# Performance work log

Measured on AMD Instinct MI355X. Metric: run time of the kernel, lower is better.

The kernel has to match this reference:

```python
import jax, jax.numpy as jnp
import numpy as np

OUT_SL = 32


def gru_cell(x, h, Wih, Whh, bih, bhh):
    # PyTorch GRU cell: gates ordered (r, z, n)
    gi = x @ Wih.T + bih
    gh = h @ Whh.T + bhh
    ir, iz, inn = jnp.split(gi, 3, axis=-1)
    hr, hz, hn = jnp.split(gh, 3, axis=-1)
    r = jax.nn.sigmoid(ir + hr)
    z = jax.nn.sigmoid(iz + hz)
    n = jnp.tanh(inn + r * hn)
    return (1.0 - z) * n + z * h


def run_gru_layer(xs, h0, Wih, Whh, bih, bhh, reverse=False):
    def step(h, x):
        h = gru_cell(x, h, Wih, Whh, bih, bhh)
        return h, h
    hT, ys = jax.lax.scan(step, h0, xs, reverse=reverse)
    return ys, hT


def setup_inputs() -> dict:
    key = jax.random.key(0)
    ks = iter(jax.random.split(key, 32))

    def p(shape, fan_in):
        return (jax.random.normal(next(ks), shape, dtype=jnp.float32)
                / np.sqrt(fan_in).astype(np.float32))

    V_ENC, V_DEC, EE, ED, NH = 32000, 32000, 300, 300, 256
    inp = jax.random.randint(next(ks), (128, 64), 0, V_ENC)
    return {
        'emb_enc': p((V_ENC, EE), 1.0),
        'enc_Wih0': p((2, 3 * NH, EE), EE),
        'enc_Whh0': p((2, 3 * NH, NH), NH),
        'enc_bih0': p((2, 3 * NH), NH),
        'enc_bhh0': p((2, 3 * NH), NH),
        'enc_Wih1': p((2, 3 * NH, 2 * NH), 2 * NH),
        'enc_Whh1': p((2, 3 * NH, NH), NH),
        'enc_bih1': p((2, 3 * NH), NH),
        'enc_bhh1': p((2, 3 * NH), NH),
        'W_out_enc': p((ED, 2 * NH), 2 * NH),
        'emb_dec': p((V_DEC, ED), 1.0),
        'dec_Wih': p((2, 3 * ED, ED), ED),
        'dec_Whh': p((2, 3 * ED, ED), ED),
        'dec_bih': p((2, 3 * ED), ED),
        'dec_bhh': p((2, 3 * ED), ED),
        'W1': p((2 * NH, ED), 2 * NH),
        'l2_W': p((ED, ED), ED),
        'l2_b': p((ED,), ED),
        'l3_W': p((ED, ED + 2 * NH), ED + 2 * NH),
        'l3_b': p((ED,), ED),
        'V_att': p((ED,), ED),
        'out_b': p((V_DEC,), ED),
        'inp': inp,
    }


def reference(emb_enc, enc_Wih0, enc_Whh0, enc_bih0, enc_bhh0,
              enc_Wih1, enc_Whh1, enc_bih1, enc_bhh1, W_out_enc,
              emb_dec, dec_Wih, dec_Whh, dec_bih, dec_bhh,
              W1, l2_W, l2_b, l3_W, l3_b, V_att, out_b, inp):
    sl, bs = inp.shape
    nh = enc_Whh0.shape[-1]
    h0 = jnp.zeros((bs, nh), dtype=emb_enc.dtype)

    # ---- encoder: 2-layer bidirectional GRU (dropout in eval mode = identity)
    emb = emb_enc[inp]                                        # (sl, bs, EE)
    yf0, hf0 = run_gru_layer(emb, h0, enc_Wih0[0], enc_Whh0[0], enc_bih0[0], enc_bhh0[0])
    yb0, hb0 = run_gru_layer(emb, h0, enc_Wih0[1], enc_Whh0[1], enc_bih0[1], enc_bhh0[1], reverse=True)
    x1 = jnp.concatenate([yf0, yb0], axis=-1)                 # (sl, bs, 2*nh)
    yf1, hf1 = run_gru_layer(x1, h0, enc_Wih1[0], enc_Whh1[0], enc_bih1[0], enc_bhh1[0])
    yb1, hb1 = run_gru_layer(x1, h0, enc_Wih1[1], enc_Whh1[1], enc_bih1[1], enc_bhh1[1], reverse=True)
    enc_out = jnp.concatenate([yf1, yb1], axis=-1)            # (sl, bs, 2*nh)

    # h.view(2,2,bs,-1).permute(0,2,1,3) -> concat fwd/bwd per layer
    h = jnp.stack([jnp.concatenate([hf0, hb0], axis=-1),
                   jnp.concatenate([hf1, hb1], axis=-1)])     # (2, bs, 2*nh)
    h = h @ W_out_enc.T                                       # (2, bs, ED)

    w1e = enc_out @ W1                                        # (sl, bs, ED)
    dec_inp0 = jnp.zeros((bs,), dtype=jnp.int32)

    def dec_step(carry, _):
        h, dec_inp = carry
        w2h = h[-1] @ l2_W.T + l2_b                           # (bs, ED)
        u = jnp.tanh(w1e + w2h[None])                         # (sl, bs, ED)
        a = jax.nn.softmax(u @ V_att, axis=0)                 # (sl, bs), softmax over seq
        Xa = jnp.einsum('sb,sbd->bd', a, enc_out)             # (bs, 2*nh)
        e = emb_dec[dec_inp]                                  # (bs, ED)
        x = jnp.concatenate([e, Xa], axis=1) @ l3_W.T + l3_b  # (bs, ED)
        h0n = gru_cell(x, h[0], dec_Wih[0], dec_Whh[0], dec_bih[0], dec_bhh[0])
        h1n = gru_cell(h0n, h[1], dec_Wih[1], dec_Whh[1], dec_bih[1], dec_bhh[1])
        outp = h1n @ emb_dec.T + out_b                        # (bs, V_dec), tied weights
        ndec = jnp.argmax(outp, axis=1).astype(jnp.int32)
        return (jnp.stack([h0n, h1n]), ndec), outp

    (_, _), res = jax.lax.scan(dec_step, (h, dec_inp0), None, length=OUT_SL)
    return res                                                # (out_sl, bs, V_dec)
```

## Files before the change

kernel.cpp:

```cpp
#include <hip/hip_runtime.h>
#include <math.h>


#define DINL static __device__ __forceinline__

DINL float sigm(float x) { return 1.0f / (1.0f + expf(-x)); }
DINL float dot4f(float4 a, float4 b) { return a.x*b.x + a.y*b.y + a.z*b.z + a.w*b.w; }

__global__ __launch_bounds__(256) void k_embed(const float4* __restrict__ E,
                                               const int* __restrict__ inp,
                                               float4* __restrict__ out) {
  int i = blockIdx.x * 256 + threadIdx.x;
  if (i >= 8192 * 75) return;
  int row = i / 75, q = i - row * 75;
  out[i] = E[(size_t)inp[row] * 75 + q];
}

__global__ __launch_bounds__(256) void k_transpose(const float* __restrict__ A,
                                                   float* __restrict__ B, int R, int C) {
  __shared__ float tile[32][33];
  int c0 = blockIdx.x * 32, r0 = blockIdx.y * 32;
  int tx = threadIdx.x & 31, ty = threadIdx.x >> 5;
  for (int i = 0; i < 32; i += 8) {
    int r = r0 + ty + i, c = c0 + tx;
    if (r < R && c < C) tile[ty + i][tx] = A[(size_t)r * C + c];
  }
  __syncthreads();
  for (int i = 0; i < 32; i += 8) {
    int c = c0 + ty + i, r = r0 + tx;
    if (c < C && r < R) B[(size_t)c * R + r] = tile[tx][ty + i];
  }
}

__global__ __launch_bounds__(256) void k_gemm_nt(const float* __restrict__ A,
                                                 const float* __restrict__ B,
                                                 const float* __restrict__ bias,
                                                 float* __restrict__ C,
                                                 int N, int M, int K) {
  __shared__ float As[16][65];
  __shared__ float Bs[16][65];
  const int tid = threadIdx.x;
  const int bn = blockIdx.x * 64, bm = blockIdx.y * 64;
  const int tn = (tid >> 4) << 2, tm = (tid & 15) << 2;
  float acc[4][4] = {};
  for (int k0 = 0; k0 < K; k0 += 16) {
    for (int i = tid; i < 1024; i += 256) {
      int kk = i & 15, n = i >> 4;
      int gk = k0 + kk;
      As[kk][n] = (gk < K) ? A[(size_t)(bn + n) * K + gk] : 0.0f;
      Bs[kk][n] = (gk < K && (bm + n) < M) ? B[(size_t)(bm + n) * K + gk] : 0.0f;
    }
    __syncthreads();
#pragma unroll
    for (int kk = 0; kk < 16; ++kk) {
      float a[4], bb[4];
#pragma unroll
      for (int i = 0; i < 4; ++i) a[i] = As[kk][tn + i];
#pragma unroll
      for (int j = 0; j < 4; ++j) bb[j] = Bs[kk][tm + j];
#pragma unroll
      for (int i = 0; i < 4; ++i)
#pragma unroll
        for (int j = 0; j < 4; ++j) acc[i][j] += a[i] * bb[j];
    }
    __syncthreads();
  }
#pragma unroll
  for (int i = 0; i < 4; ++i) {
    int row = bn + tn + i;
#pragma unroll
    for (int j = 0; j < 4; ++j) {
      int col = bm + tm + j;
      if (row < N && col < M)
        C[(size_t)row * M + col] = acc[i][j] + (bias ? bias[col] : 0.0f);
    }
  }
}

__global__ __launch_bounds__(256) void k_enc_step(
    const float* __restrict__ giF, const float* __restrict__ giB,
    const float* __restrict__ hinF, const float* __restrict__ hinB,
    float* __restrict__ houtF, float* __restrict__ houtB,
    const float* __restrict__ WhhF, const float* __restrict__ WhhB,
    const float* __restrict__ bhhF, const float* __restrict__ bhhB,
    float* __restrict__ yF, float* __restrict__ yB) {
  const int dir = blockIdx.z;
  const float* gi = dir ? giB : giF;
  const float* hin = dir ? hinB : hinF;
  float* hout = dir ? houtB : houtF;
  const float* Whh = dir ? WhhB : WhhF;
  const float* bhh = dir ? bhhB : bhhF;
  float* y = dir ? yB : yF;
  const int ycol = dir ? 256 : 0;

  const int c0 = blockIdx.x * 16;
  const int b0 = blockIdx.y * 16;
  const int tid = threadIdx.x;
  const int cl = tid & 15, bl = tid >> 4;

  __shared__ __align__(16) float Wlds[3][16][260];
  for (int i = tid; i < 48 * 64; i += 256) {
    int row = i >> 6, q = i & 63;
    int g = row >> 4, rc = row & 15;
    float4 w = ((const float4*)Whh)[(size_t)(c0 + rc + (g << 8)) * 64 + q];
    *(float4*)&Wlds[g][rc][q << 2] = w;
  }
  __syncthreads();

  const int b = b0 + bl;
  const int c = c0 + cl;
  const float* hrow = hin + (b << 8);
  float ar = 0.f, az = 0.f, an = 0.f;
#pragma unroll 4
  for (int k = 0; k < 256; k += 4) {
    float4 hv = *(const float4*)(hrow + k);
    float4 wr = *(const float4*)&Wlds[0][cl][k];
    float4 wz = *(const float4*)&Wlds[1][cl][k];
    float4 wn = *(const float4*)&Wlds[2][cl][k];
    ar += dot4f(hv, wr);
    az += dot4f(hv, wz);
    an += dot4f(hv, wn);
  }
  float ghr = ar + bhh[c], ghz = az + bhh[256 + c], ghn = an + bhh[512 + c];
  const float* gir = gi + (size_t)b * 768;
  float r = sigm(gir[c] + ghr);
  float z = sigm(gir[256 + c] + ghz);
  float n = tanhf(gir[512 + c] + r * ghn);
  float hold = hrow[c];
  float hnew = (1.f - z) * n + z * hold;
  hout[(b << 8) + c] = hnew;
  y[(b << 9) + ycol + c] = hnew;
}

__global__ __launch_bounds__(256) void k_hcat(const float* __restrict__ x1,
                                              const float* __restrict__ encout,
                                              float* __restrict__ hcat) {
  int i = blockIdx.x * 256 + threadIdx.x;
  int l = i >> 15, r = i & 32767, b = r >> 9, d = r & 511;
  const float* src = l ? encout : x1;
  int ts = (d < 256) ? 127 : 0;
  hcat[i] = src[((size_t)(ts << 6) + b) * 512 + d];
}

__global__ __launch_bounds__(256) void k_dec_att(
    const float* __restrict__ h1, const float* __restrict__ w1e,
    const float* __restrict__ encout,
    const float* __restrict__ l2W, const float* __restrict__ l2b,
    const float* __restrict__ l3W, const float* __restrict__ l3b,
    const float* __restrict__ Vatt, const float* __restrict__ embdec,
    const int* __restrict__ decin, float* __restrict__ xdec) {
  const int b = blockIdx.x, tid = threadIdx.x;
  __shared__ __align__(16) float h1s[300];
  __shared__ __align__(16) float w2h[300];
  __shared__ __align__(16) float eXa[812];
  __shared__ float aa[128];
  __shared__ float red[128];

  for (int i = tid; i < 300; i += 256) h1s[i] = h1[b * 300 + i];
  __syncthreads();

  for (int m = tid; m < 300; m += 256) {
    const float4* wr = (const float4*)(l2W + (size_t)m * 300);
    const float4* hr = (const float4*)h1s;
    float acc = l2b[m];
    for (int q = 0; q < 75; ++q) acc += dot4f(wr[q], hr[q]);
    w2h[m] = acc;
  }
  __syncthreads();

  if (tid < 128) {
    const float4* wp = (const float4*)(w1e + ((size_t)(tid << 6) + b) * 300);
    const float4* vp = (const float4*)Vatt;
    const float4* hp = (const float4*)w2h;
    float acc = 0.f;
    for (int q = 0; q < 75; ++q) {
      float4 w = wp[q], h = hp[q], v = vp[q];
      acc += tanhf(w.x + h.x) * v.x + tanhf(w.y + h.y) * v.y +
             tanhf(w.z + h.z) * v.z + tanhf(w.w + h.w) * v.w;
    }
    aa[tid] = acc;
    red[tid] = acc;
  }
  __syncthreads();
  for (int s = 64; s > 0; s >>= 1) {
    if (tid < s) red[tid] = fmaxf(red[tid], red[tid + s]);
    __syncthreads();
  }
  float mx = red[0];
  __syncthreads();
  if (tid < 128) {
    float ex = expf(aa[tid] - mx);
    aa[tid] = ex;
    red[tid] = ex;
  }
  __syncthreads();
  for (int s = 64; s > 0; s >>= 1) {
    if (tid < s) red[tid] += red[tid + s];
    __syncthreads();
  }
  float inv = 1.0f / red[0];
  __syncthreads();
  if (tid < 128) aa[tid] *= inv;
  int ib = decin[b];
  for (int d = tid; d < 300; d += 256) eXa[d] = embdec[(size_t)ib * 300 + d];
  __syncthreads();

  for (int d = tid; d < 512; d += 256) {
    float acc = 0.f;
    for (int s = 0; s < 128; ++s) acc += aa[s] * encout[((size_t)(s << 6) + b) * 512 + d];
    eXa[300 + d] = acc;
  }
  __syncthreads();

  for (int m = tid; m < 300; m += 256) {
    const float4* wr = (const float4*)(l3W + (size_t)m * 812);
    const float4* xr = (const float4*)eXa;
    float acc = l3b[m];
    for (int q = 0; q < 203; ++q) acc += dot4f(wr[q], xr[q]);
    xdec[b * 300 + m] = acc;
  }
}

__global__ __launch_bounds__(256) void k_gru300(
    const float* __restrict__ xin, const float* __restrict__ hin,
    float* __restrict__ hout, float* __restrict__ houtT,
    const float* __restrict__ Wih, const float* __restrict__ Whh,
    const float* __restrict__ bih, const float* __restrict__ bhh) {
  const int tid = threadIdx.x;
  const int cl = tid & 15, bl = tid >> 4;
  const int c = blockIdx.x * 16 + cl;
  const int b0 = blockIdx.y * 16;
  const int b = b0 + bl;
  __shared__ __align__(16) float xs[16][300];
  __shared__ __align__(16) float hs[16][300];
  for (int i = tid; i < 16 * 75; i += 256) {
    int row = i / 75, q = i - row * 75;
    ((float4*)&xs[row][0])[q] = ((const float4*)(xin + (size_t)(b0 + row) * 300))[q];
    ((float4*)&hs[row][0])[q] = ((const float4*)(hin + (size_t)(b0 + row) * 300))[q];
  }
  __syncthreads();
  if (c < 300) {
    float gir = bih[c], giz = bih[300 + c], gin = bih[600 + c];
    float ghr = bhh[c], ghz = bhh[300 + c], ghn = bhh[600 + c];
    const float4* wir = (const float4*)(Wih + (size_t)c * 300);
    const float4* wiz = (const float4*)(Wih + (size_t)(300 + c) * 300);
    const float4* win = (const float4*)(Wih + (size_t)(600 + c) * 300);
    const float4* whr = (const float4*)(Whh + (size_t)c * 300);
    const float4* whz = (const float4*)(Whh + (size_t)(300 + c) * 300);
    const float4* whn = (const float4*)(Whh + (size_t)(600 + c) * 300);
    const float4* xr = (const float4*)&xs[bl][0];
    const float4* hr = (const float4*)&hs[bl][0];
    for (int q = 0; q < 75; ++q) {
      float4 xv = xr[q], hv = hr[q];
      gir += dot4f(xv, wir[q]);
      giz += dot4f(xv, wiz[q]);
      gin += dot4f(xv, win[q]);
      ghr += dot4f(hv, whr[q]);
      ghz += dot4f(hv, whz[q]);
      ghn += dot4f(hv, whn[q]);
    }
    float r = sigm(gir + ghr), z = sigm(giz + ghz);
    float n = tanhf(gin + r * ghn);
    float hnew = (1.f - z) * n + z * hs[bl][c];
    hout[(size_t)b * 300 + c] = hnew;
    if (houtT) houtT[(size_t)c * 64 + b] = hnew;
  }
}

__global__ __launch_bounds__(256) void k_dec_out(const float* __restrict__ embT,
                                                 const float* __restrict__ h1T,
                                                 const float* __restrict__ outb,
                                                 float* __restrict__ out) {
  const int v = blockIdx.x * 256 + threadIdx.x;
  const int bh = blockIdx.y;
  const float* h = h1T + bh * 32;
  float acc[32];
#pragma unroll
  for (int i = 0; i < 32; ++i) acc[i] = 0.f;
  for (int k = 0; k < 300; ++k) {
    float ev = embT[(size_t)k * 32000 + v];
#pragma unroll
    for (int i = 0; i < 32; ++i) acc[i] += ev * h[(size_t)k * 64 + i];
  }
  float bo = outb[v];
#pragma unroll
  for (int i = 0; i < 32; ++i) out[(size_t)(bh * 32 + i) * 32000 + v] = acc[i] + bo;
}

__global__ __launch_bounds__(256) void k_argmax(const float* __restrict__ out,
                                                int* __restrict__ decin) {
  const int b = blockIdx.x, tid = threadIdx.x;
  const float* row = out + (size_t)b * 32000;
  float best = -INFINITY;
  int bi = 0;
  for (int v = tid; v < 32000; v += 256) {
    float x = row[v];
    if (x > best) { best = x; bi = v; }
  }
  __shared__ float bv[256];
  __shared__ int bidx[256];
  bv[tid] = best;
  bidx[tid] = bi;
  __syncthreads();
  for (int s = 128; s > 0; s >>= 1) {
    if (tid < s) {
      if (bv[tid + s] > bv[tid] || (bv[tid + s] == bv[tid] && bidx[tid + s] < bidx[tid])) {
        bv[tid] = bv[tid + s];
        bidx[tid] = bidx[tid + s];
      }
    }
    __syncthreads();
  }
  if (tid == 0) decin[b] = bidx[0];
}

extern "C" void kernel_launch(void* const* d_in, const int* in_sizes, int n_in,
                              void* d_out_v, int out_size, void* d_ws, size_t ws_size,
                              hipStream_t stream) {
  (void)in_sizes; (void)n_in; (void)out_size; (void)ws_size;
  const float* emb_enc = (const float*)d_in[0];
  const float* eWih0   = (const float*)d_in[1];
  const float* eWhh0   = (const float*)d_in[2];
  const float* ebih0   = (const float*)d_in[3];
  const float* ebhh0   = (const float*)d_in[4];
  const float* eWih1   = (const float*)d_in[5];
  const float* eWhh1   = (const float*)d_in[6];
  const float* ebih1   = (const float*)d_in[7];
  const float* ebhh1   = (const float*)d_in[8];
  const float* Wout    = (const float*)d_in[9];
  const float* emb_dec = (const float*)d_in[10];
  const float* dWih    = (const float*)d_in[11];
  const float* dWhh    = (const float*)d_in[12];
  const float* dbih    = (const float*)d_in[13];
  const float* dbhh    = (const float*)d_in[14];
  const float* W1      = (const float*)d_in[15];
  const float* l2W     = (const float*)d_in[16];
  const float* l2b     = (const float*)d_in[17];
  const float* l3W     = (const float*)d_in[18];
  const float* l3b     = (const float*)d_in[19];
  const float* Vatt    = (const float*)d_in[20];
  const float* outb    = (const float*)d_in[21];
  const int* inp       = (const int*)d_in[22];
  float* d_out = (float*)d_out_v;

  float* ws = (float*)d_ws;
  size_t off = 0;
  auto take = [&](size_t n) { float* p = ws + off; off += (n + 3) & ~(size_t)3; return p; };
  float* embT   = take((size_t)300 * 32000);
  float* encout = take((size_t)8192 * 512);
  float* w1e    = take((size_t)8192 * 300);
  float* W1T    = take((size_t)300 * 512);
  float* hcat   = take((size_t)128 * 512);
  float* dech   = take((size_t)2 * 2 * 64 * 300);
  float* h1T    = take((size_t)300 * 64);
  float* xdec   = take((size_t)64 * 300);
  float* henc   = take((size_t)4 * 64 * 256);
  int* decin    = (int*)take(64);

  float* emb  = d_out;
  float* gi0f = emb + 2457600;
  float* gi0b = gi0f + 6291456;
  float* x1   = gi0b + 6291456;
  float* gi1f = x1 + 4194304;
  float* gi1b = gi1f + 6291456;

  k_embed<<<2400, 256, 0, stream>>>((const float4*)emb_enc, inp, (float4*)emb);
  k_transpose<<<dim3(10, 16), 256, 0, stream>>>(W1, W1T, 512, 300);
  k_transpose<<<dim3(10, 1000), 256, 0, stream>>>(emb_dec, embT, 32000, 300);

  k_gemm_nt<<<dim3(128, 12), 256, 0, stream>>>(emb, eWih0, ebih0, gi0f, 8192, 768, 300);
  k_gemm_nt<<<dim3(128, 12), 256, 0, stream>>>(emb, eWih0 + 230400, ebih0 + 768, gi0b, 8192, 768, 300);
  hipMemsetAsync(henc, 0, 4 * 64 * 256 * sizeof(float), stream);
  for (int t = 0; t < 128; ++t) {
    int tb = 127 - t, pp = t & 1, np = pp ^ 1;
    k_enc_step<<<dim3(16, 4, 2), 256, 0, stream>>>(
        gi0f + (size_t)t * 49152, gi0b + (size_t)tb * 49152,
        henc + (pp * 2 + 0) * 16384, henc + (pp * 2 + 1) * 16384,
        henc + (np * 2 + 0) * 16384, henc + (np * 2 + 1) * 16384,
        eWhh0, eWhh0 + 196608, ebhh0, ebhh0 + 768,
        x1 + (size_t)t * 32768, x1 + (size_t)tb * 32768);
  }

  k_gemm_nt<<<dim3(128, 12), 256, 0, stream>>>(x1, eWih1, ebih1, gi1f, 8192, 768, 512);
  k_gemm_nt<<<dim3(128, 12), 256, 0, stream>>>(x1, eWih1 + 393216, ebih1 + 768, gi1b, 8192, 768, 512);
  hipMemsetAsync(henc, 0, 4 * 64 * 256 * sizeof(float), stream);
  for (int t = 0; t < 128; ++t) {
    int tb = 127 - t, pp = t & 1, np = pp ^ 1;
    k_enc_step<<<dim3(16, 4, 2), 256, 0, stream>>>(
        gi1f + (size_t)t * 49152, gi1b + (size_t)tb * 49152,
        henc + (pp * 2 + 0) * 16384, henc + (pp * 2 + 1) * 16384,
        henc + (np * 2 + 0) * 16384, henc + (np * 2 + 1) * 16384,
        eWhh1, eWhh1 + 196608, ebhh1, ebhh1 + 768,
        encout + (size_t)t * 32768, encout + (size_t)tb * 32768);
  }

  k_hcat<<<256, 256, 0, stream>>>(x1, encout, hcat);
  k_gemm_nt<<<dim3(2, 5), 256, 0, stream>>>(hcat, Wout, nullptr, dech, 128, 300, 512);
  k_gemm_nt<<<dim3(128, 5), 256, 0, stream>>>(encout, W1T, nullptr, w1e, 8192, 300, 512);

  hipMemsetAsync(decin, 0, 64 * sizeof(int), stream);
  for (int t = 0; t < 32; ++t) {
    int cur = t & 1, nxt = cur ^ 1;
    float* hc = dech + cur * 38400;
    float* hn = dech + nxt * 38400;
    k_dec_att<<<64, 256, 0, stream>>>(hc + 19200, w1e, encout, l2W, l2b, l3W, l3b,
                                      Vatt, emb_dec, decin, xdec);
    k_gru300<<<dim3(19, 4), 256, 0, stream>>>(xdec, hc, hn, nullptr,
                                              dWih, dWhh, dbih, dbhh);
    k_gru300<<<dim3(19, 4), 256, 0, stream>>>(hn, hc + 19200, hn + 19200, h1T,
                                              dWih + 270000, dWhh + 270000,
                                              dbih + 900, dbhh + 900);
    k_dec_out<<<dim3(125, 2), 256, 0, stream>>>(embT, h1T, outb,
                                                d_out + (size_t)t * 2048000);
    k_argmax<<<64, 256, 0, stream>>>(d_out + (size_t)t * 2048000, decin);
  }
}
```

Baseline: 11.22 ms.

## Persistent encoder recurrence with grid barriers, larger GEMM tiles, fused argmax

Replaces 128 per-timestep encoder launches per layer with one persistent kernel per layer. Blocks sharing a batch slice synchronise each step through atomic counters in global memory. The input-projection GEMM moves to 128x128 tiles with 8x8 register blocking, and the separate argmax kernel is folded into the output projection via packed 64-bit max keys reduced in the next attention kernel. This removes launch overhead and a full re-read of the logits, but relies on all 128 blocks being co-resident, which spin barriers require.

```diff
diff --git a/kernel.cpp b/kernel.cpp
--- a/kernel.cpp
+++ b/kernel.cpp
@@ -6,6 +6,15 @@
 
 DINL float sigm(float x) { return 1.0f / (1.0f + expf(-x)); }
 DINL float dot4f(float4 a, float4 b) { return a.x*b.x + a.y*b.y + a.z*b.z + a.w*b.w; }
+
+DINL unsigned long long packmax(float x, int v) {
+  unsigned u = __float_as_uint(x);
+  u = (u & 0x80000000u) ? ~u : (u | 0x80000000u);
+  return ((unsigned long long)u << 32) | (unsigned)(~v);
+}
+DINL unsigned long long umax64(unsigned long long a, unsigned long long b) {
+  return a > b ? a : b;
+}
 
 __global__ __launch_bounds__(256) void k_embed(const float4* __restrict__ E,
                                                const int* __restrict__ inp,
@@ -32,104 +41,123 @@
   }
 }
 
-__global__ __launch_bounds__(256) void k_gemm_nt(const float* __restrict__ A,
+__global__ __launch_bounds__(256) void k_gemm128(const float* __restrict__ A,
                                                  const float* __restrict__ B,
                                                  const float* __restrict__ bias,
                                                  float* __restrict__ C,
                                                  int N, int M, int K) {
-  __shared__ float As[16][65];
-  __shared__ float Bs[16][65];
+  __shared__ float As[8][132];
+  __shared__ float Bs[8][132];
   const int tid = threadIdx.x;
-  const int bn = blockIdx.x * 64, bm = blockIdx.y * 64;
-  const int tn = (tid >> 4) << 2, tm = (tid & 15) << 2;
-  float acc[4][4] = {};
-  for (int k0 = 0; k0 < K; k0 += 16) {
-    for (int i = tid; i < 1024; i += 256) {
-      int kk = i & 15, n = i >> 4;
-      int gk = k0 + kk;
-      As[kk][n] = (gk < K) ? A[(size_t)(bn + n) * K + gk] : 0.0f;
-      Bs[kk][n] = (gk < K && (bm + n) < M) ? B[(size_t)(bm + n) * K + gk] : 0.0f;
-    }
+  const int bn = blockIdx.x * 128, bm = blockIdx.y * 128;
+  const int tn = (tid >> 4) << 3, tm = (tid & 15) << 3;
+  const int r = tid & 127;
+  const bool isB = tid >= 128;
+  const float* src = isB ? (B + (size_t)(bm + r) * K) : (A + (size_t)(bn + r) * K);
+  const bool rowok = isB ? (bm + r < M) : (bn + r < N);
+  float acc[8][8] = {};
+  for (int k0 = 0; k0 < K; k0 += 8) {
+    float v[8];
+    if (rowok && k0 + 8 <= K) {
+      float4 p0 = *(const float4*)(src + k0);
+      float4 p1 = *(const float4*)(src + k0 + 4);
+      v[0]=p0.x; v[1]=p0.y; v[2]=p0.z; v[3]=p0.w;
+      v[4]=p1.x; v[5]=p1.y; v[6]=p1.z; v[7]=p1.w;
+    } else {
+#pragma unroll
+      for (int j = 0; j < 8; ++j) v[j] = (rowok && k0 + j < K) ? src[k0 + j] : 0.0f;
+    }
+    float (*dst)[132] = isB ? Bs : As;
+#pragma unroll
+    for (int j = 0; j < 8; ++j) dst[j][r] = v[j];
     __syncthreads();
 #pragma unroll
-    for (int kk = 0; kk < 16; ++kk) {
-      float a[4], bb[4];
-#pragma unroll
-      for (int i = 0; i < 4; ++i) a[i] = As[kk][tn + i];
-#pragma unroll
-      for (int j = 0; j < 4; ++j) bb[j] = Bs[kk][tm + j];
-#pragma unroll
-      for (int i = 0; i < 4; ++i)
-#pragma unroll
-        for (int j = 0; j < 4; ++j) acc[i][j] += a[i] * bb[j];
+    for (int kk = 0; kk < 8; ++kk) {
+      float a[8], b[8];
+      *(float4*)&a[0] = *(const float4*)&As[kk][tn];
+      *(float4*)&a[4] = *(const float4*)&As[kk][tn + 4];
+      *(float4*)&b[0] = *(const float4*)&Bs[kk][tm];
+      *(float4*)&b[4] = *(const float4*)&Bs[kk][tm + 4];
+#pragma unroll
+      for (int i = 0; i < 8; ++i)
+#pragma unroll
+        for (int j = 0; j < 8; ++j) acc[i][j] += a[i] * b[j];
     }
     __syncthreads();
   }
 #pragma unroll
-  for (int i = 0; i < 4; ++i) {
+  for (int i = 0; i < 8; ++i) {
     int row = bn + tn + i;
-#pragma unroll
-    for (int j = 0; j < 4; ++j) {
+    if (row >= N) continue;
+#pragma unroll
+    for (int j = 0; j < 8; ++j) {
       int col = bm + tm + j;
-      if (row < N && col < M)
-        C[(size_t)row * M + col] = acc[i][j] + (bias ? bias[col] : 0.0f);
-    }
-  }
-}
-
-__global__ __launch_bounds__(256) void k_enc_step(
+      if (col < M) C[(size_t)row * M + col] = acc[i][j] + (bias ? bias[col] : 0.0f);
+    }
+  }
+}
+
+__global__ __launch_bounds__(256) void k_enc_layer(
     const float* __restrict__ giF, const float* __restrict__ giB,
-    const float* __restrict__ hinF, const float* __restrict__ hinB,
-    float* __restrict__ houtF, float* __restrict__ houtB,
-    const float* __restrict__ WhhF, const float* __restrict__ WhhB,
-    const float* __restrict__ bhhF, const float* __restrict__ bhhB,
-    float* __restrict__ yF, float* __restrict__ yB) {
+    const float* __restrict__ Whh,
+    const float* __restrict__ bhh,
+    float* __restrict__ y,
+    float* __restrict__ hbuf,
+    int* __restrict__ bar) {
   const int dir = blockIdx.z;
+  const int c0 = blockIdx.x * 16, b0 = blockIdx.y * 16;
+  const int tid = threadIdx.x, cl = tid & 15, bl = tid >> 4;
   const float* gi = dir ? giB : giF;
-  const float* hin = dir ? hinB : hinF;
-  float* hout = dir ? houtB : houtF;
-  const float* Whh = dir ? WhhB : WhhF;
-  const float* bhh = dir ? bhhB : bhhF;
-  float* y = dir ? yB : yF;
-  const int ycol = dir ? 256 : 0;
-
-  const int c0 = blockIdx.x * 16;
-  const int b0 = blockIdx.y * 16;
-  const int tid = threadIdx.x;
-  const int cl = tid & 15, bl = tid >> 4;
+  const float* W = Whh + (size_t)dir * 196608;
+  const float* bh = bhh + dir * 768;
+  float* hb = hbuf + dir * 16384;
+  int* mybar = bar + (dir * 4 + blockIdx.y) * 128;
 
   __shared__ __align__(16) float Wlds[3][16][260];
   for (int i = tid; i < 48 * 64; i += 256) {
     int row = i >> 6, q = i & 63;
     int g = row >> 4, rc = row & 15;
-    float4 w = ((const float4*)Whh)[(size_t)(c0 + rc + (g << 8)) * 64 + q];
+    float4 w = ((const float4*)W)[(size_t)(c0 + rc + (g << 8)) * 64 + q];
     *(float4*)&Wlds[g][rc][q << 2] = w;
   }
   __syncthreads();
 
-  const int b = b0 + bl;
-  const int c = c0 + cl;
-  const float* hrow = hin + (b << 8);
-  float ar = 0.f, az = 0.f, an = 0.f;
+  const int b = b0 + bl, c = c0 + cl;
+  const float bhr = bh[c], bhz = bh[256 + c], bhn = bh[512 + c];
+
+  for (int t = 0; t < 128; ++t) {
+    const int tt = dir ? 127 - t : t;
+    const int pp = t & 1;
+    const float* hrow = hb + pp * 32768 + (b << 8);
+    float ar = 0.f, az = 0.f, an = 0.f;
 #pragma unroll 4
-  for (int k = 0; k < 256; k += 4) {
-    float4 hv = *(const float4*)(hrow + k);
-    float4 wr = *(const float4*)&Wlds[0][cl][k];
-    float4 wz = *(const float4*)&Wlds[1][cl][k];
-    float4 wn = *(const float4*)&Wlds[2][cl][k];
-    ar += dot4f(hv, wr);
-    az += dot4f(hv, wz);
-    an += dot4f(hv, wn);
-  }
-  float ghr = ar + bhh[c], ghz = az + bhh[256 + c], ghn = an + bhh[512 + c];
-  const float* gir = gi + (size_t)b * 768;
-  float r = sigm(gir[c] + ghr);
-  float z = sigm(gir[256 + c] + ghz);
-  float n = tanhf(gir[512 + c] + r * ghn);
-  float hold = hrow[c];
-  float hnew = (1.f - z) * n + z * hold;
-  hout[(b << 8) + c] = hnew;
-  y[(b << 9) + ycol + c] = hnew;
+    for (int k = 0; k < 256; k += 4) {
+      float4 hv = *(const float4*)(hrow + k);
+      float4 wr = *(const float4*)&Wlds[0][cl][k];
+      float4 wz = *(const float4*)&Wlds[1][cl][k];
+      float4 wn = *(const float4*)&Wlds[2][cl][k];
+      ar += dot4f(hv, wr);
+      az += dot4f(hv, wz);
+      an += dot4f(hv, wn);
+    }
+    const float* gir = gi + (size_t)tt * 49152 + (size_t)b * 768;
+    float rg = sigm(gir[c] + ar + bhr);
+    float zg = sigm(gir[256 + c] + az + bhz);
+    float ng = tanhf(gir[512 + c] + rg * (an + bhn));
+    float hnew = (1.f - zg) * ng + zg * hrow[c];
+    hb[(pp ^ 1) * 32768 + (b << 8) + c] = hnew;
+    y[(size_t)tt * 32768 + (b << 9) + (dir << 8) + c] = hnew;
+
+    if (t < 127) {
+      __syncthreads();
+      if (tid == 0) {
+        __hip_atomic_fetch_add(&mybar[t], 1, __ATOMIC_RELEASE, __HIP_MEMORY_SCOPE_AGENT);
+        while (__hip_atomic_load(&mybar[t], __ATOMIC_ACQUIRE, __HIP_MEMORY_SCOPE_AGENT) < 16)
+          __builtin_amdgcn_s_sleep(1);
+      }
+      __syncthreads();
+    }
+  }
 }
 
 __global__ __launch_bounds__(256) void k_hcat(const float* __restrict__ x1,
@@ -148,16 +176,24 @@
     const float* __restrict__ l2W, const float* __restrict__ l2b,
     const float* __restrict__ l3W, const float* __restrict__ l3b,
     const float* __restrict__ Vatt, const float* __restrict__ embdec,
-    const int* __restrict__ decin, float* __restrict__ xdec) {
+    const unsigned long long* __restrict__ prev,
+    float* __restrict__ xdec) {
   const int b = blockIdx.x, tid = threadIdx.x;
   __shared__ __align__(16) float h1s[300];
   __shared__ __align__(16) float w2h[300];
   __shared__ __align__(16) float eXa[812];
   __shared__ float aa[128];
   __shared__ float red[128];
-
+  __shared__ unsigned long long redb[128];
+
+  if (tid < 128) redb[tid] = (prev && tid < 125) ? prev[(size_t)tid * 64 + b] : 0ULL;
   for (int i = tid; i < 300; i += 256) h1s[i] = h1[b * 300 + i];
   __syncthreads();
+  for (int s = 64; s > 0; s >>= 1) {
+    if (tid < s) redb[tid] = umax64(redb[tid], redb[tid + s]);
+    __syncthreads();
+  }
+  const int ib = prev ? (int)(~(unsigned)(redb[0] & 0xFFFFFFFFULL)) : 0;
 
   for (int m = tid; m < 300; m += 256) {
     const float4* wr = (const float4*)(l2W + (size_t)m * 300);
@@ -201,7 +237,6 @@
   float inv = 1.0f / red[0];
   __syncthreads();
   if (tid < 128) aa[tid] *= inv;
-  int ib = decin[b];
   for (int d = tid; d < 300; d += 256) eXa[d] = embdec[(size_t)ib * 300 + d];
   __syncthreads();
 
@@ -270,10 +305,14 @@
 __global__ __launch_bounds__(256) void k_dec_out(const float* __restrict__ embT,
                                                  const float* __restrict__ h1T,
                                                  const float* __restrict__ outb,
-                                                 float* __restrict__ out) {
-  const int v = blockIdx.x * 256 + threadIdx.x;
+                                                 float* __restrict__ out,
+                                                 unsigned long long* __restrict__ bests) {
+  const int tid = threadIdx.x;
+  const int v = blockIdx.x * 256 + tid;
   const int bh = blockIdx.y;
   const float* h = h1T + bh * 32;
+  __shared__ float accs[32][257];
+  __shared__ unsigned long long red[256];
   float acc[32];
 #pragma unroll
   for (int i = 0; i < 32; ++i) acc[i] = 0.f;
@@ -284,34 +323,26 @@
   }
   float bo = outb[v];
 #pragma unroll
-  for (int i = 0; i < 32; ++i) out[(size_t)(bh * 32 + i) * 32000 + v] = acc[i] + bo;
-}
-
-__global__ __launch_bounds__(256) void k_argmax(const float* __restrict__ out,
-                                                int* __restrict__ decin) {
-  const int b = blockIdx.x, tid = threadIdx.x;
-  const float* row = out + (size_t)b * 32000;
-  float best = -INFINITY;
-  int bi = 0;
-  for (int v = tid; v < 32000; v += 256) {
-    float x = row[v];
-    if (x > best) { best = x; bi = v; }
-  }
-  __shared__ float bv[256];
-  __shared__ int bidx[256];
-  bv[tid] = best;
-  bidx[tid] = bi;
-  __syncthreads();
-  for (int s = 128; s > 0; s >>= 1) {
-    if (tid < s) {
-      if (bv[tid + s] > bv[tid] || (bv[tid + s] == bv[tid] && bidx[tid + s] < bidx[tid])) {
-        bv[tid] = bv[tid + s];
-        bidx[tid] = bidx[tid + s];
-      }
-    }
-    __syncthreads();
-  }
-  if (tid == 0) decin[b] = bidx[0];
+  for (int i = 0; i < 32; ++i) {
+    float val = acc[i] + bo;
+    out[(size_t)(bh * 32 + i) * 32000 + v] = val;
+    accs[i][tid] = val;
+  }
+  __syncthreads();
+  const int i2 = tid >> 3, j = tid & 7;
+  unsigned long long best = 0ULL;
+  for (int k = 0; k < 32; ++k) {
+    int cc = (j << 5) | k;
+    best = umax64(best, packmax(accs[i2][cc], (blockIdx.x << 8) | cc));
+  }
+  red[tid] = best;
+  __syncthreads();
+  if (tid < 32) {
+    unsigned long long m = red[tid << 3];
+#pragma unroll
+    for (int k = 1; k < 8; ++k) m = umax64(m, red[(tid << 3) | k]);
+    bests[(size_t)blockIdx.x * 64 + (bh << 5) + tid] = m;
+  }
 }
 
 extern "C" void kernel_launch(void* const* d_in, const int* in_sizes, int n_in,
@@ -354,8 +385,9 @@
   float* dech   = take((size_t)2 * 2 * 64 * 300);
   float* h1T    = take((size_t)300 * 64);
   float* xdec   = take((size_t)64 * 300);
-  float* henc   = take((size_t)4 * 64 * 256);
-  int* decin    = (int*)take(64);
+  float* hbuf   = take((size_t)2 * 2 * 64 * 256);
+  unsigned long long* bests = (unsigned long long*)take((size_t)125 * 64 * 2);
+  int* bar      = (int*)take((size_t)2 * 8 * 128);
 
   float* emb  = d_out;
   float* gi0f = emb + 2457600;
@@ -364,54 +396,38 @@
   float* gi1f = x1 + 4194304;
   float* gi1b = gi1f + 6291456;
 
+  hipMemsetAsync(bar, 0, 2 * 8 * 128 * sizeof(int), stream);
+
   k_embed<<<2400, 256, 0, stream>>>((const float4*)emb_enc, inp, (float4*)emb);
   k_transpose<<<dim3(10, 16), 256, 0, stream>>>(W1, W1T, 512, 300);
   k_transpose<<<dim3(10, 1000), 256, 0, stream>>>(emb_dec, embT, 32000, 300);
 
-  k_gemm_nt<<<dim3(128, 12), 256, 0, stream>>>(emb, eWih0, ebih0, gi0f, 8192, 768, 300);
-  k_gemm_nt<<<dim3(128, 12), 256, 0, stream>>>(emb, eWih0 + 230400, ebih0 + 768, gi0b, 8192, 768, 300);
-  hipMemsetAsync(henc, 0, 4 * 64 * 256 * sizeof(float), stream);
-  for (int t = 0; t < 128; ++t) {
-    int tb = 127 - t, pp = t & 1, np = pp ^ 1;
-    k_enc_step<<<dim3(16, 4, 2), 256, 0, stream>>>(
-        gi0f + (size_t)t * 49152, gi0b + (size_t)tb * 49152,
-        henc + (pp * 2 + 0) * 16384, henc + (pp * 2 + 1) * 16384,
-        henc + (np * 2 + 0) * 16384, henc + (np * 2 + 1) * 16384,
-        eWhh0, eWhh0 + 196608, ebhh0, ebhh0 + 768,
-        x1 + (size_t)t * 32768, x1 + (size_t)tb * 32768);
-  }
-
-  k_gemm_nt<<<dim3(128, 12), 256, 0, stream>>>(x1, eWih1, ebih1, gi1f, 8192, 768, 512);
-  k_gemm_nt<<<dim3(128, 12), 256, 0, stream>>>(x1, eWih1 + 393216, ebih1 + 768, gi1b, 8192, 768, 512);
-  hipMemsetAsync(henc, 0, 4 * 64 * 256 * sizeof(float), stream);
-  for (int t = 0; t < 128; ++t) {
-    int tb = 127 - t, pp = t & 1, np = pp ^ 1;
-    k_enc_step<<<dim3(16, 4, 2), 256, 0, stream>>>(
-        gi1f + (size_t)t * 49152, gi1b + (size_t)tb * 49152,
-        henc + (pp * 2 + 0) * 16384, henc + (pp * 2 + 1) * 16384,
-        henc + (np * 2 + 0) * 16384, henc + (np * 2 + 1) * 16384,
-        eWhh1, eWhh1 + 196608, ebhh1, ebhh1 + 768,
-        encout + (size_t)t * 32768, encout + (size_t)tb * 32768);
-  }
+  k_gemm128<<<dim3(64, 6), 256, 0, stream>>>(emb, eWih0, ebih0, gi0f, 8192, 768, 300);
+  k_gemm128<<<dim3(64, 6), 256, 0, stream>>>(emb, eWih0 + 230400, ebih0 + 768, gi0b, 8192, 768, 300);
+  hipMemsetAsync(hbuf, 0, 2 * 2 * 64 * 256 * sizeof(float), stream);
+  k_enc_layer<<<dim3(16, 4, 2), 256, 0, stream>>>(gi0f, gi0b, eWhh0, ebhh0, x1, hbuf, bar);
+
+  k_gemm128<<<dim3(64, 6), 256, 0, stream>>>(x1, eWih1, ebih1, gi1f, 8192, 768, 512);
+  k_gemm128<<<dim3(64, 6), 256, 0, stream>>>(x1, eWih1 + 393216, ebih1 + 768, gi1b, 8192, 768, 512);
+  hipMemsetAsync(hbuf, 0, 2 * 2 * 64 * 256 * sizeof(float), stream);
+  k_enc_layer<<<dim3(16, 4, 2), 256, 0, stream>>>(gi1f, gi1b, eWhh1, ebhh1, encout, hbuf, bar + 1024);
 
   k_hcat<<<256, 256, 0, stream>>>(x1, encout, hcat);
-  k_gemm_nt<<<dim3(2, 5), 256, 0, stream>>>(hcat, Wout, nullptr, dech, 128, 300, 512);
-  k_gemm_nt<<<dim3(128, 5), 256, 0, stream>>>(encout, W1T, nullptr, w1e, 8192, 300, 512);
-
-  hipMemsetAsync(decin, 0, 64 * sizeof(int), stream);
+  k_gemm128<<<dim3(1, 3), 256, 0, stream>>>(hcat, Wout, nullptr, dech, 128, 300, 512);
+  k_gemm128<<<dim3(64, 3), 256, 0, stream>>>(encout, W1T, nullptr, w1e, 8192, 300, 512);
+
   for (int t = 0; t < 32; ++t) {
     int cur = t & 1, nxt = cur ^ 1;
     float* hc = dech + cur * 38400;
     float* hn = dech + nxt * 38400;
     k_dec_att<<<64, 256, 0, stream>>>(hc + 19200, w1e, encout, l2W, l2b, l3W, l3b,
-                                      Vatt, emb_dec, decin, xdec);
+                                      Vatt, emb_dec, t ? bests : nullptr, xdec);
     k_gru300<<<dim3(19, 4), 256, 0, stream>>>(xdec, hc, hn, nullptr,
                                               dWih, dWhh, dbih, dbhh);
     k_gru300<<<dim3(19, 4), 256, 0, stream>>>(hn, hc + 19200, hn + 19200, h1T,
                                               dWih + 270000, dWhh + 270000,
                                               dbih + 900, dbhh + 900);
     k_dec_out<<<dim3(125, 2), 256, 0, stream>>>(embT, h1T, outb,
-                                                d_out + (size_t)t * 2048000);
-    k_argmax<<<64, 256, 0, stream>>>(d_out + (size_t)t * 2048000, decin);
-  }
-}
+                                                d_out + (size_t)t * 2048000, bests);
+  }
+}
```

Result: faster. 10.34 ms (-7.8%).
